# Kernel optimization log

Hardware: AMD Instinct MI355X
Metric: run time of the kernel (lower is better)

## Reference

```python
import jax, jax.numpy as jnp
import numpy as np

HIDDEN = 300
ATOM_FDIM = 133
BOND_ONLY_FDIM = 14
BOND_FDIM = ATOM_FDIM + BOND_ONLY_FDIM  # 147, chemprop concatenates atom feats into bond feats
DEPTH = 3
N_ATOMS = 100000
N_BONDS = 200000  # directed bonds, stored as reverse pairs (2k, 2k+1)
MAX_NB = 6
N_MOLS = 2000


def _lin(key, fan_in, fan_out):
    s = 1.0 / np.sqrt(fan_in)
    return jax.random.uniform(key, (fan_in, fan_out), jnp.float32, -s, s)


def setup_inputs() -> dict:
    key = jax.random.key(0)
    ks = jax.random.split(key, 16)
    f_atoms = jax.random.normal(ks[0], (N_ATOMS, ATOM_FDIM), jnp.float32)
    f_bonds = jax.random.normal(ks[1], (N_BONDS, BOND_FDIM), jnp.float32)
    a2b = jax.random.randint(ks[2], (N_ATOMS, MAX_NB), 0, N_BONDS, jnp.int32)
    b2a = jax.random.randint(ks[3], (N_BONDS,), 0, N_ATOMS, jnp.int32)
    b2revb = jnp.arange(N_BONDS, dtype=jnp.int32) ^ 1  # reverse-bond pairing
    graph_idx = jnp.sort(jax.random.randint(ks[4], (N_ATOMS,), 0, N_MOLS, jnp.int32))
    params = dict(
        W_i=_lin(ks[5], BOND_FDIM, HIDDEN),              # no bias in chemprop W_i
        W_h=_lin(ks[6], HIDDEN, HIDDEN),                 # no bias in chemprop W_h
        W_o=_lin(ks[7], ATOM_FDIM + HIDDEN, HIDDEN),
        b_o=jnp.zeros((HIDDEN,), jnp.float32),
        W_node=_lin(ks[8], HIDDEN, ATOM_FDIM),
        b_node=jnp.zeros((ATOM_FDIM,), jnp.float32),
        W_edge=_lin(ks[9], HIDDEN, BOND_ONLY_FDIM),
        b_edge=jnp.zeros((BOND_ONLY_FDIM,), jnp.float32),
        W_g1=_lin(ks[10], HIDDEN, HIDDEN),
        b_g1=jnp.zeros((HIDDEN,), jnp.float32),
        W_g2=_lin(ks[11], HIDDEN, 1),
        b_g2=jnp.zeros((1,), jnp.float32),
    )
    return dict(f_atoms=f_atoms, f_bonds=f_bonds, a2b=a2b, b2a=b2a,
                b2revb=b2revb, graph_idx=graph_idx, **params)


def reference(f_atoms, f_bonds, a2b, b2a, b2revb, graph_idx,
              W_i, W_h, W_o, b_o, W_node, b_node,
              W_edge, b_edge, W_g1, b_g1, W_g2, b_g2):
    # ---- chemprop bond-message MPN encoder (dropout=0) ----
    inp = f_bonds @ W_i                       # [n_bonds, H]
    msg = jax.nn.relu(inp)
    for _ in range(DEPTH - 1):
        a_msg = msg[a2b].sum(axis=1)          # gather neighbor bond msgs -> [n_atoms, H]
        msg = jax.nn.relu(inp + (a_msg[b2a] - msg[b2revb]) @ W_h)
    a_msg = msg[a2b].sum(axis=1)
    atom_hiddens = jax.nn.relu(jnp.concatenate([f_atoms, a_msg], axis=-1) @ W_o + b_o)
    # ---- graph pooling: per-molecule SUM (as in the forward loop) ----
    graph_emb = jax.ops.segment_sum(atom_hiddens, graph_idx, num_segments=N_MOLS)
    # ---- heads ----
    node_preds = atom_hiddens @ W_node + b_node
    # bond loop: visits each reverse pair once (even bond first), averages endpoint atoms
    e1 = jnp.arange(0, N_BONDS, 2)
    a1 = b2a[e1]
    a2 = b2a[b2revb[e1]]
    h_avg = 0.5 * (atom_hiddens[a1] + atom_hiddens[a2])
    edge_preds = h_avg @ W_edge + b_edge
    graph_preds = jax.nn.relu(graph_emb @ W_g1 + b_g1) @ W_g2 + b_g2
    return node_preds, edge_preds, graph_preds
```

## Files before the change

kernel.cpp:

```cpp
#include <hip/hip_runtime.h>

typedef unsigned short u16;
typedef unsigned int u32;

#define N_ATOMS 100000
#define N_BONDS 200000
#define N_EDGES 100000
#define HIDDEN 300
#define HP 320
#define ATOM_FDIM 133
#define BOND_FDIM 147
#define CATP 448
#define N_MOLS 2000

typedef __bf16 bf16x8 __attribute__((ext_vector_type(8)));
typedef float f32x4 __attribute__((ext_vector_type(4)));

__device__ __forceinline__ u16 f2bf(float f) {
    union { float f; u32 u; } x; x.f = f;
    u32 u = x.u;
    u32 r = u + 0x7fffu + ((u >> 16) & 1u);
    return (u16)(r >> 16);
}
__device__ __forceinline__ float bf2f(u16 h) {
    union { u32 u; float f; } x; x.u = ((u32)h) << 16;
    return x.f;
}

union U8 { uint4 v; u16 h[8]; };
union U4 { uint2 v; u16 h[4]; };

template<int ASRC, int EP, int KSTEPS>
__global__ __launch_bounds__(256, 4) void k_gemm_lds(
    const float* __restrict__ fsrc, const u16* __restrict__ src16,
    const u16* __restrict__ src16b, const int* __restrict__ i1,
    const int* __restrict__ i2, int lda, int M,
    const u16* __restrict__ Bt, int ldb,
    int Nout, float* __restrict__ Cf, int ldc,
    const float* __restrict__ bias, u16* __restrict__ O1,
    const u16* __restrict__ inp_in)
{
    constexpr int CHPR = KSTEPS * 4;
    constexpr int MASK = (CHPR % 8 == 0) ? 7 : 3;
    __shared__ __align__(16) u16 As[32 * CHPR * 8];

    const int tid = threadIdx.x;
    const int row0 = blockIdx.x * 32;

    constexpr int TOT = 32 * CHPR;
    constexpr int ITER = (TOT + 255) / 256;
#pragma unroll
    for (int it = 0; it < ITER; it++) {
        int ch = tid + it * 256;
        if (TOT % 256 != 0 && ch >= TOT) break;
        int r = ch / CHPR, c = ch - r * CHPR;
        int row = row0 + r; if (row >= M) row = M - 1;
        U8 u;
        if constexpr (ASRC == 1) {
            size_t fb = (size_t)row * lda;
#pragma unroll
            for (int e = 0; e < 8; e++) {
                int col = c * 8 + e;
                u.h[e] = (col < lda) ? f2bf(fsrc[fb + col]) : (u16)0;
            }
        } else if constexpr (ASRC == 2) {
            U8 x, y;
            x.v = *(const uint4*)(src16  + (size_t)i1[row] * HP + c * 8);
            y.v = *(const uint4*)(src16b + (size_t)i2[row] * HP + c * 8);
#pragma unroll
            for (int e = 0; e < 8; e++)
                u.h[e] = f2bf(bf2f(x.h[e]) - fmaxf(bf2f(y.h[e]), 0.f));
        } else {
            if (c < 38) {
                u.v = *(const uint4*)(src16 + (size_t)row * HP + c * 8);
            } else {
                size_t fb = (size_t)row * ATOM_FDIM;
#pragma unroll
                for (int e = 0; e < 8; e++) {
                    int col = c * 8 + e - 304;
                    u.h[e] = (col >= 0 && col < ATOM_FDIM) ? f2bf(fsrc[fb + col]) : (u16)0;
                }
            }
        }
        *(uint4*)&As[(size_t)(r * CHPR + (c ^ (r & MASK))) * 8] = u.v;
    }
    __syncthreads();

    const int lane = tid & 63;
    const int w = tid >> 6;
    const int ncol0 = w * 80;
    const int lrow = lane & 15;
    const int g = lane >> 4;
    const int lkb = g * 8;
    const int xr = lrow & MASK;

    const u16* pb[5];
#pragma unroll
    for (int n = 0; n < 5; n++)
        pb[n] = Bt + (size_t)(ncol0 + n * 16 + lrow) * ldb + lkb;

    f32x4 acc[2][5] = {};
    bf16x8 bcur[5], bnxt[5];
#pragma unroll
    for (int n = 0; n < 5; n++) bcur[n] = *(const bf16x8*)(pb[n]);

#pragma unroll
    for (int ks = 0; ks < KSTEPS; ks++) {
        if (ks + 1 < KSTEPS) {
#pragma unroll
            for (int n = 0; n < 5; n++) bnxt[n] = *(const bf16x8*)(pb[n] + (ks + 1) * 32);
        }
        const int sw = (ks * 4 + g) ^ xr;
        bf16x8 a0 = *(const bf16x8*)&As[(size_t)(lrow * CHPR + sw) * 8];
        bf16x8 a1 = *(const bf16x8*)&As[(size_t)((lrow + 16) * CHPR + sw) * 8];
#pragma unroll
        for (int n = 0; n < 5; n++) {
            acc[0][n] = __builtin_amdgcn_mfma_f32_16x16x32_bf16(bcur[n], a0, acc[0][n], 0, 0, 0);
            acc[1][n] = __builtin_amdgcn_mfma_f32_16x16x32_bf16(bcur[n], a1, acc[1][n], 0, 0, 0);
        }
#pragma unroll
        for (int n = 0; n < 5; n++) bcur[n] = bnxt[n];
    }

#pragma unroll
    for (int m = 0; m < 2; m++) {
        const int row = row0 + m * 16 + lrow;
#pragma unroll
        for (int n = 0; n < 5; n++) {
            const int colb = ncol0 + n * 16 + g * 4;
            U4 o;
            if constexpr (EP == 1) {
#pragma unroll
                for (int q = 0; q < 4; q++) o.h[q] = f2bf(acc[m][n][q]);
            } else if constexpr (EP == 2) {
                U4 ii; ii.v = *(const uint2*)&inp_in[(size_t)row * HP + colb];
#pragma unroll
                for (int q = 0; q < 4; q++) o.h[q] = f2bf(acc[m][n][q] + bf2f(ii.h[q]));
            } else {
#pragma unroll
                for (int q = 0; q < 4; q++) {
                    float x = acc[m][n][q] + ((colb + q) < Nout ? bias[colb + q] : 0.f);
                    o.h[q] = f2bf(fmaxf(x, 0.f));
                }
            }
            *(uint2*)&O1[(size_t)row * HP + colb] = o.v;
        }
    }
}

template<int ASRC, int EP, int KSTEPS, int NFW, int WAVEM>
__global__ __launch_bounds__(256) void k_gemm(
    const float* __restrict__ fsrc, const u16* __restrict__ src16,
    const u16* __restrict__ src16b, const int* __restrict__ i1,
    const int* __restrict__ i2, int lda, int M,
    const u16* __restrict__ Bt, int ldb,
    int Nout, float* __restrict__ Cf, int ldc,
    const float* __restrict__ bias, u16* __restrict__ O1,
    const u16* __restrict__ inp_in)
{
    const int tid = threadIdx.x;
    const int lane = tid & 63;
    const int w = tid >> 6;
    const int lrow = lane & 15;
    const int lkb = (lane >> 4) * 8;

    int row0, ncol0;
    if constexpr (WAVEM) { row0 = blockIdx.x * 128 + w * 32; ncol0 = 0; }
    else                 { row0 = blockIdx.x * 32;           ncol0 = w * (NFW * 16); }

    const u16* pa[2] = {nullptr, nullptr};
    const u16* pa2[2] = {nullptr, nullptr};
#pragma unroll
    for (int m = 0; m < 2; m++) {
        int r = row0 + m * 16 + lrow; if (r >= M) r = M - 1;
        if constexpr (ASRC == 0) pa[m] = src16 + (size_t)r * lda + lkb;
        if constexpr (ASRC == 4) {
            int e = 2 * r;
            pa[m]  = src16 + (size_t)i1[e] * HP + lkb;
            pa2[m] = src16 + (size_t)i1[i2[e]] * HP + lkb;
        }
    }

    const u16* pb[NFW];
#pragma unroll
    for (int n = 0; n < NFW; n++)
        pb[n] = Bt + (size_t)(ncol0 + n * 16 + lrow) * ldb + lkb;

    auto loadAfrag = [&](int m, int k0) -> bf16x8 {
        U8 u;
        if constexpr (ASRC == 0) {
            u.v = *(const uint4*)(pa[m] + k0);
        } else {
            U8 x, y; x.v = *(const uint4*)(pa[m] + k0); y.v = *(const uint4*)(pa2[m] + k0);
#pragma unroll
            for (int e = 0; e < 8; e++)
                u.h[e] = f2bf(0.5f * (bf2f(x.h[e]) + bf2f(y.h[e])));
        }
        return *(bf16x8*)&u;
    };

    f32x4 acc[2][NFW] = {};

#pragma unroll
    for (int ks = 0; ks < KSTEPS; ks++) {
        const int k0 = ks * 32;
        bf16x8 a0 = loadAfrag(0, k0);
        bf16x8 a1 = loadAfrag(1, k0);
        bf16x8 bfr[NFW];
#pragma unroll
        for (int n = 0; n < NFW; n++) bfr[n] = *(const bf16x8*)(pb[n] + k0);
#pragma unroll
        for (int n = 0; n < NFW; n++) {
            acc[0][n] = __builtin_amdgcn_mfma_f32_16x16x32_bf16(a0, bfr[n], acc[0][n], 0, 0, 0);
            acc[1][n] = __builtin_amdgcn_mfma_f32_16x16x32_bf16(a1, bfr[n], acc[1][n], 0, 0, 0);
        }
    }

    const int orow = (lane >> 4) * 4;
    const int ocol = lane & 15;
#pragma unroll
    for (int m = 0; m < 2; m++) {
#pragma unroll
        for (int n = 0; n < NFW; n++) {
#pragma unroll
            for (int q = 0; q < 4; q++) {
                int grow = row0 + m * 16 + orow + q;
                int gcol = ncol0 + n * 16 + ocol;
                float v = acc[m][n][q];
                if constexpr (EP == 0) {
                    if (grow < M && gcol < Nout)
                        Cf[(size_t)grow * ldc + gcol] = v + bias[gcol];
                } else {
                    if (grow < M) O1[(size_t)grow * HP + gcol] = f2bf(v);
                }
            }
        }
    }
}

__global__ void k_pack_wt(const float* __restrict__ W, u16* __restrict__ Bt,
                          int K, int N, int Kp, int Np)
{
    int idx = blockIdx.x * 256 + threadIdx.x;
    if (idx >= Np * Kp) return;
    int n = idx / Kp, k = idx - n * Kp;
    Bt[idx] = (n < N && k < K) ? f2bf(W[(size_t)k * N + n]) : (u16)0;
}

__global__ void k_pack_wo(const float* __restrict__ W, u16* __restrict__ Bt)
{
    int idx = blockIdx.x * 256 + threadIdx.x;
    if (idx >= 320 * CATP) return;
    int n = idx / CATP, k = idx - n * CATP;
    float v = 0.f;
    if (n < HIDDEN) {
        if (k < HIDDEN) v = W[(size_t)(ATOM_FDIM + k) * HIDDEN + n];
        else if (k >= 304 && k < 304 + ATOM_FDIM) v = W[(size_t)(k - 304) * HIDDEN + n];
    }
    Bt[idx] = f2bf(v);
}

__global__ __launch_bounds__(256) void k_aggregate(const u16* __restrict__ h,
    const int* __restrict__ a2b, u16* __restrict__ amsg)
{
    int idx = blockIdx.x * 256 + threadIdx.x;
    if (idx >= N_ATOMS * 40) return;
    int a = idx / 40, c = (idx - a * 40) * 8;
    float s[8] = {};
#pragma unroll
    for (int j = 0; j < 6; j++) {
        int b = a2b[a * 6 + j];
        U8 u; u.v = *(const uint4*)&h[(size_t)b * HP + c];
#pragma unroll
        for (int i = 0; i < 8; i++) s[i] += fmaxf(bf2f(u.h[i]), 0.f);
    }
    U8 o;
#pragma unroll
    for (int i = 0; i < 8; i++) o.h[i] = f2bf(s[i]);
    *(uint4*)&amsg[(size_t)a * HP + c] = o.v;
}

__device__ __forceinline__ int lower_bound_i(const int* a, int n, int v) {
    int lo = 0, hi = n;
    while (lo < hi) { int mid = (lo + hi) >> 1; if (a[mid] < v) lo = mid + 1; else hi = mid; }
    return lo;
}
__global__ __launch_bounds__(320) void k_segsum(const u16* __restrict__ ah,
    const int* __restrict__ gidx, float* __restrict__ gemb)
{
    int g = blockIdx.x;
    int c = threadIdx.x;
    int s = lower_bound_i(gidx, N_ATOMS, g);
    int e = lower_bound_i(gidx, N_ATOMS, g + 1);
    float sum = 0.f;
    for (int a = s; a < e; a++) sum += bf2f(ah[(size_t)a * HP + c]);
    gemb[(size_t)g * HP + c] = sum;
}

__global__ __launch_bounds__(320) void k_g1(const float* __restrict__ gemb,
    const float* __restrict__ W, const float* __restrict__ b, float* __restrict__ gh)
{
    int g = blockIdx.x, j = threadIdx.x;
    float acc = 0.f;
    if (j < HIDDEN) {
        acc = b[j];
        for (int k = 0; k < HIDDEN; k++)
            acc = fmaf(gemb[(size_t)g * HP + k], W[(size_t)k * HIDDEN + j], acc);
        acc = fmaxf(acc, 0.f);
    }
    gh[(size_t)g * HP + j] = (j < HIDDEN) ? acc : 0.f;
}
__global__ __launch_bounds__(64) void k_g2(const float* __restrict__ gh,
    const float* __restrict__ W, const float* __restrict__ b, float* __restrict__ out)
{
    int g = blockIdx.x, l = threadIdx.x;
    float acc = 0.f;
    for (int j = l; j < HIDDEN; j += 64) acc += gh[(size_t)g * HP + j] * W[j];
#pragma unroll
    for (int off = 32; off; off >>= 1) acc += __shfl_down(acc, off, 64);
    if (l == 0) out[g] = acc + b[0];
}

extern "C" void kernel_launch(void* const* d_in, const int* in_sizes, int n_in,
                              void* d_out, int out_size, void* d_ws, size_t ws_size,
                              hipStream_t stream)
{
    const float* f_atoms = (const float*)d_in[0];
    const float* f_bonds = (const float*)d_in[1];
    const int* a2b    = (const int*)d_in[2];
    const int* b2a    = (const int*)d_in[3];
    const int* b2revb = (const int*)d_in[4];
    const int* gidx   = (const int*)d_in[5];
    const float* W_i    = (const float*)d_in[6];
    const float* W_h    = (const float*)d_in[7];
    const float* W_o    = (const float*)d_in[8];
    const float* b_o    = (const float*)d_in[9];
    const float* W_node = (const float*)d_in[10];
    const float* b_node = (const float*)d_in[11];
    const float* W_edge = (const float*)d_in[12];
    const float* b_edge = (const float*)d_in[13];
    const float* W_g1   = (const float*)d_in[14];
    const float* b_g1   = (const float*)d_in[15];
    const float* W_g2   = (const float*)d_in[16];
    const float* b_g2   = (const float*)d_in[17];

    char* ws = (char*)d_ws;
    u16* inp  = (u16*)(ws + 0);
    u16* hA   = (u16*)(ws + 128000000);
    u16* hB   = (u16*)(ws + 256000000);
    u16* amsg = (u16*)(ws + 384000000);
    u16* wt_i = (u16*)(ws + 448000000);
    u16* wt_h = (u16*)(ws + 448200000);
    u16* wt_o = (u16*)(ws + 448500000);
    u16* wt_n = (u16*)(ws + 448800000);
    u16* wt_e = (u16*)(ws + 449000000);
    float* gemb = (float*)(ws + 449300000);
    float* gh   = (float*)(ws + 452000000);

    float* out_node  = (float*)d_out;
    float* out_edge  = out_node + (size_t)N_ATOMS * ATOM_FDIM;
    float* out_graph = out_node + 14700000;

    dim3 blk(256);

    k_pack_wt<<<(320 * 160 + 255) / 256, blk, 0, stream>>>(W_i, wt_i, BOND_FDIM, HIDDEN, 160, 320);
    k_pack_wt<<<(320 * 320 + 255) / 256, blk, 0, stream>>>(W_h, wt_h, HIDDEN, HIDDEN, 320, 320);
    k_pack_wo<<<(320 * CATP + 255) / 256, blk, 0, stream>>>(W_o, wt_o);
    k_pack_wt<<<(192 * 320 + 255) / 256, blk, 0, stream>>>(W_node, wt_n, HIDDEN, ATOM_FDIM, 320, 192);
    k_pack_wt<<<(64 * 320 + 255) / 256, blk, 0, stream>>>(W_edge, wt_e, HIDDEN, 14, 320, 64);

    const int gB32 = (N_BONDS + 31) / 32;
    const int gA32 = (N_ATOMS + 31) / 32;
    const int gE128 = (N_EDGES + 127) / 128;
    const int gAg = (N_ATOMS * 40 + 255) / 256;

    k_gemm_lds<1, 1, 5><<<gB32, blk, 0, stream>>>(
        f_bonds, nullptr, nullptr, nullptr, nullptr, BOND_FDIM, N_BONDS,
        wt_i, 160, 0, nullptr, 0, nullptr, inp, nullptr);

    const u16* hcur = inp;
    u16* houts[2] = { hA, hB };
    for (int d = 0; d < 2; ++d) {
        k_aggregate<<<gAg, blk, 0, stream>>>(hcur, a2b, amsg);
        k_gemm_lds<2, 2, 10><<<gB32, blk, 0, stream>>>(
            nullptr, amsg, hcur, b2a, b2revb, 0, N_BONDS,
            wt_h, 320, 0, nullptr, 0, nullptr, houts[d], inp);
        hcur = houts[d];
    }

    k_aggregate<<<gAg, blk, 0, stream>>>(hcur, a2b, amsg);
    u16* ah = hA;
    k_gemm_lds<3, 3, 14><<<gA32, blk, 0, stream>>>(
        f_atoms, amsg, nullptr, nullptr, nullptr, 0, N_ATOMS,
        wt_o, CATP, HIDDEN, nullptr, 0, b_o, ah, nullptr);

    k_gemm<0, 0, 10, 3, 0><<<gA32, blk, 0, stream>>>(
        nullptr, ah, nullptr, nullptr, nullptr, HP, N_ATOMS,
        wt_n, 320, ATOM_FDIM, out_node, ATOM_FDIM, b_node, nullptr, nullptr);

    k_gemm<4, 0, 10, 1, 1><<<gE128, blk, 0, stream>>>(
        nullptr, ah, nullptr, b2a, b2revb, 0, N_EDGES,
        wt_e, 320, 14, out_edge, 14, b_edge, nullptr, nullptr);

    k_segsum<<<N_MOLS, 320, 0, stream>>>(ah, gidx, gemb);
    k_g1<<<N_MOLS, 320, 0, stream>>>(gemb, W_g1, b_g1, gh);
    k_g2<<<N_MOLS, 64, 0, stream>>>(gh, W_g2, b_g2, out_graph);
}
```

Measured before the change: 1.150 ms.

## Warp-specialize GEMMs into persistent producer/consumer kernels with double-buffered LDS

Replaces the one-tile-per-block LDS GEMM with a persistent 512-thread kernel. Four producer waves stage the next 32-row A tile (gathers, subtract-relu) into a second LDS buffer while four MFMA waves compute the current tile, so global loads overlap with compute. To make producer loads plain vector copies, f_bonds and f_atoms are first converted to padded bf16 buffers by new pack kernels. This adds two extra full passes over the feature matrices and doubles LDS use, and with a fixed grid of 512 only one tile is ever staged ahead.

```diff
diff --git a/kernel.cpp b/kernel.cpp
--- a/kernel.cpp
+++ b/kernel.cpp
@@ -30,120 +30,157 @@
 union U8 { uint4 v; u16 h[8]; };
 union U4 { uint2 v; u16 h[4]; };
 
-template<int ASRC, int EP, int KSTEPS>
-__global__ __launch_bounds__(256, 4) void k_gemm_lds(
-    const float* __restrict__ fsrc, const u16* __restrict__ src16,
-    const u16* __restrict__ src16b, const int* __restrict__ i1,
-    const int* __restrict__ i2, int lda, int M,
-    const u16* __restrict__ Bt, int ldb,
-    int Nout, float* __restrict__ Cf, int ldc,
-    const float* __restrict__ bias, u16* __restrict__ O1,
-    const u16* __restrict__ inp_in)
+template<int ASRC, int EP, int KSTEPS, int LDA>
+__global__ __launch_bounds__(512, 4) void k_gemm_pipe(
+    const u16* __restrict__ srcA, const u16* __restrict__ srcB,
+    const int* __restrict__ i1, const int* __restrict__ i2,
+    int ntiles, const u16* __restrict__ Bt, int ldb,
+    int Nout, const float* __restrict__ bias,
+    u16* __restrict__ O1, const u16* __restrict__ inp_in)
 {
     constexpr int CHPR = KSTEPS * 4;
     constexpr int MASK = (CHPR % 8 == 0) ? 7 : 3;
-    __shared__ __align__(16) u16 As[32 * CHPR * 8];
+    constexpr int CPT = (CHPR + 7) / 8;
+    __shared__ __align__(16) u16 As[2][32 * CHPR * 8];
 
     const int tid = threadIdx.x;
-    const int row0 = blockIdx.x * 32;
-
-    constexpr int TOT = 32 * CHPR;
-    constexpr int ITER = (TOT + 255) / 256;
-#pragma unroll
-    for (int it = 0; it < ITER; it++) {
-        int ch = tid + it * 256;
-        if (TOT % 256 != 0 && ch >= TOT) break;
-        int r = ch / CHPR, c = ch - r * CHPR;
-        int row = row0 + r; if (row >= M) row = M - 1;
-        U8 u;
-        if constexpr (ASRC == 1) {
-            size_t fb = (size_t)row * lda;
-#pragma unroll
-            for (int e = 0; e < 8; e++) {
-                int col = c * 8 + e;
-                u.h[e] = (col < lda) ? f2bf(fsrc[fb + col]) : (u16)0;
+    const int wv = tid >> 6;
+    const int tile0 = blockIdx.x;
+    if (tile0 >= ntiles) return;
+
+    if (wv >= 4) {
+        const int ptid = tid - 256;
+        const int rr = ptid >> 3;
+        const int c0 = ptid & 7;
+
+        uint4 sx[CPT], sy[(ASRC == 2) ? CPT : 1];
+
+        auto stage = [&](int tile, int buf) {
+            const int row = tile * 32 + rr;
+            if constexpr (ASRC == 0) {
+                const u16* px = srcA + (size_t)row * LDA;
+#pragma unroll
+                for (int j = 0; j < CPT; j++) {
+                    int c = c0 + 8 * j;
+                    if (CHPR % 8 == 0 || c < CHPR)
+                        sx[j] = *(const uint4*)(px + c * 8);
+                }
+            } else if constexpr (ASRC == 2) {
+                const u16* px = srcA + (size_t)i1[row] * HP;
+                const u16* py = srcB + (size_t)i2[row] * HP;
+#pragma unroll
+                for (int j = 0; j < CPT; j++) {
+                    int c = c0 + 8 * j;
+                    sx[j] = *(const uint4*)(px + c * 8);
+                    sy[j] = *(const uint4*)(py + c * 8);
+                }
+            } else {
+                const u16* pa = srcA + (size_t)row * HP;
+                const u16* pf = srcB + (size_t)row * 160;
+#pragma unroll
+                for (int j = 0; j < CPT; j++) {
+                    int c = c0 + 8 * j;
+                    sx[j] = (c < 38) ? *(const uint4*)(pa + c * 8)
+                                     : *(const uint4*)(pf + (c - 38) * 8);
+                }
             }
-        } else if constexpr (ASRC == 2) {
-            U8 x, y;
-            x.v = *(const uint4*)(src16  + (size_t)i1[row] * HP + c * 8);
-            y.v = *(const uint4*)(src16b + (size_t)i2[row] * HP + c * 8);
-#pragma unroll
-            for (int e = 0; e < 8; e++)
-                u.h[e] = f2bf(bf2f(x.h[e]) - fmaxf(bf2f(y.h[e]), 0.f));
-        } else {
-            if (c < 38) {
-                u.v = *(const uint4*)(src16 + (size_t)row * HP + c * 8);
-            } else {
-                size_t fb = (size_t)row * ATOM_FDIM;
-#pragma unroll
-                for (int e = 0; e < 8; e++) {
-                    int col = c * 8 + e - 304;
-                    u.h[e] = (col >= 0 && col < ATOM_FDIM) ? f2bf(fsrc[fb + col]) : (u16)0;
-                }
+#pragma unroll
+            for (int j = 0; j < CPT; j++) {
+                int c = c0 + 8 * j;
+                if (CHPR % 8 != 0 && c >= CHPR) continue;
+                U8 u;
+                if constexpr (ASRC == 2) {
+                    U8 x, y; x.v = sx[j]; y.v = sy[j];
+#pragma unroll
+                    for (int e = 0; e < 8; e++)
+                        u.h[e] = f2bf(bf2f(x.h[e]) - fmaxf(bf2f(y.h[e]), 0.f));
+                } else {
+                    u.v = sx[j];
+                }
+                *(uint4*)&As[buf][(size_t)(rr * CHPR + (c ^ (rr & MASK))) * 8] = u.v;
             }
-        }
-        *(uint4*)&As[(size_t)(r * CHPR + (c ^ (r & MASK))) * 8] = u.v;
-    }
-    __syncthreads();
-
-    const int lane = tid & 63;
-    const int w = tid >> 6;
-    const int ncol0 = w * 80;
-    const int lrow = lane & 15;
-    const int g = lane >> 4;
-    const int lkb = g * 8;
-    const int xr = lrow & MASK;
-
-    const u16* pb[5];
-#pragma unroll
-    for (int n = 0; n < 5; n++)
-        pb[n] = Bt + (size_t)(ncol0 + n * 16 + lrow) * ldb + lkb;
-
-    f32x4 acc[2][5] = {};
-    bf16x8 bcur[5], bnxt[5];
-#pragma unroll
-    for (int n = 0; n < 5; n++) bcur[n] = *(const bf16x8*)(pb[n]);
-
-#pragma unroll
-    for (int ks = 0; ks < KSTEPS; ks++) {
-        if (ks + 1 < KSTEPS) {
-#pragma unroll
-            for (int n = 0; n < 5; n++) bnxt[n] = *(const bf16x8*)(pb[n] + (ks + 1) * 32);
-        }
-        const int sw = (ks * 4 + g) ^ xr;
-        bf16x8 a0 = *(const bf16x8*)&As[(size_t)(lrow * CHPR + sw) * 8];
-        bf16x8 a1 = *(const bf16x8*)&As[(size_t)((lrow + 16) * CHPR + sw) * 8];
-#pragma unroll
-        for (int n = 0; n < 5; n++) {
-            acc[0][n] = __builtin_amdgcn_mfma_f32_16x16x32_bf16(bcur[n], a0, acc[0][n], 0, 0, 0);
-            acc[1][n] = __builtin_amdgcn_mfma_f32_16x16x32_bf16(bcur[n], a1, acc[1][n], 0, 0, 0);
-        }
-#pragma unroll
-        for (int n = 0; n < 5; n++) bcur[n] = bnxt[n];
-    }
-
-#pragma unroll
-    for (int m = 0; m < 2; m++) {
-        const int row = row0 + m * 16 + lrow;
-#pragma unroll
-        for (int n = 0; n < 5; n++) {
-            const int colb = ncol0 + n * 16 + g * 4;
-            U4 o;
-            if constexpr (EP == 1) {
-#pragma unroll
-                for (int q = 0; q < 4; q++) o.h[q] = f2bf(acc[m][n][q]);
-            } else if constexpr (EP == 2) {
-                U4 ii; ii.v = *(const uint2*)&inp_in[(size_t)row * HP + colb];
-#pragma unroll
-                for (int q = 0; q < 4; q++) o.h[q] = f2bf(acc[m][n][q] + bf2f(ii.h[q]));
-            } else {
-#pragma unroll
-                for (int q = 0; q < 4; q++) {
-                    float x = acc[m][n][q] + ((colb + q) < Nout ? bias[colb + q] : 0.f);
-                    o.h[q] = f2bf(fmaxf(x, 0.f));
-                }
+        };
+
+        stage(tile0, 0);
+        __syncthreads();
+        int cur = 0;
+        for (int tile = tile0;;) {
+            int nxt = tile + gridDim.x;
+            if (nxt >= ntiles) break;
+            stage(nxt, cur ^ 1);
+            __syncthreads();
+            cur ^= 1; tile = nxt;
+        }
+    } else {
+        const int lane = tid & 63;
+        const int ncol0 = wv * 80;
+        const int lrow = lane & 15;
+        const int g = lane >> 4;
+        const int lkb = g * 8;
+        const int xr = lrow & MASK;
+
+        const u16* pb[5];
+#pragma unroll
+        for (int n = 0; n < 5; n++)
+            pb[n] = Bt + (size_t)(ncol0 + n * 16 + lrow) * ldb + lkb;
+
+        auto compute = [&](int tile, int buf) {
+            f32x4 acc[2][5] = {};
+            bf16x8 bcur[5], bnxt[5];
+#pragma unroll
+            for (int n = 0; n < 5; n++) bcur[n] = *(const bf16x8*)(pb[n]);
+#pragma unroll
+            for (int ks = 0; ks < KSTEPS; ks++) {
+                if (ks + 1 < KSTEPS) {
+#pragma unroll
+                    for (int n = 0; n < 5; n++) bnxt[n] = *(const bf16x8*)(pb[n] + (ks + 1) * 32);
+                }
+                const int sw = (ks * 4 + g) ^ xr;
+                bf16x8 a0 = *(const bf16x8*)&As[buf][(size_t)(lrow * CHPR + sw) * 8];
+                bf16x8 a1 = *(const bf16x8*)&As[buf][(size_t)((lrow + 16) * CHPR + sw) * 8];
+#pragma unroll
+                for (int n = 0; n < 5; n++) {
+                    acc[0][n] = __builtin_amdgcn_mfma_f32_16x16x32_bf16(bcur[n], a0, acc[0][n], 0, 0, 0);
+                    acc[1][n] = __builtin_amdgcn_mfma_f32_16x16x32_bf16(bcur[n], a1, acc[1][n], 0, 0, 0);
+                }
+#pragma unroll
+                for (int n = 0; n < 5; n++) bcur[n] = bnxt[n];
             }
-            *(uint2*)&O1[(size_t)row * HP + colb] = o.v;
+            const int row0 = tile * 32;
+#pragma unroll
+            for (int m = 0; m < 2; m++) {
+                const int row = row0 + m * 16 + lrow;
+#pragma unroll
+                for (int n = 0; n < 5; n++) {
+                    const int colb = ncol0 + n * 16 + g * 4;
+                    U4 o;
+                    if constexpr (EP == 1) {
+#pragma unroll
+                        for (int q = 0; q < 4; q++) o.h[q] = f2bf(acc[m][n][q]);
+                    } else if constexpr (EP == 2) {
+                        U4 ii; ii.v = *(const uint2*)&inp_in[(size_t)row * HP + colb];
+#pragma unroll
+                        for (int q = 0; q < 4; q++) o.h[q] = f2bf(acc[m][n][q] + bf2f(ii.h[q]));
+                    } else {
+#pragma unroll
+                        for (int q = 0; q < 4; q++) {
+                            float x = acc[m][n][q] + ((colb + q) < Nout ? bias[colb + q] : 0.f);
+                            o.h[q] = f2bf(fmaxf(x, 0.f));
+                        }
+                    }
+                    *(uint2*)&O1[(size_t)row * HP + colb] = o.v;
+                }
+            }
+        };
+
+        __syncthreads();
+        int cur = 0;
+        for (int tile = tile0;;) {
+            int nxt = tile + gridDim.x;
+            compute(tile, cur);
+            if (nxt >= ntiles) break;
+            __syncthreads();
+            cur ^= 1; tile = nxt;
         }
     }
 }
@@ -258,6 +295,22 @@
         else if (k >= 304 && k < 304 + ATOM_FDIM) v = W[(size_t)(k - 304) * HIDDEN + n];
     }
     Bt[idx] = f2bf(v);
+}
+
+__global__ void k_pack_bonds(const float* __restrict__ fb, u16* __restrict__ out)
+{
+    int idx = blockIdx.x * 256 + threadIdx.x;
+    if (idx >= N_BONDS * 160) return;
+    int b = idx / 160, c = idx - b * 160;
+    out[idx] = (c < BOND_FDIM) ? f2bf(fb[(size_t)b * BOND_FDIM + c]) : (u16)0;
+}
+
+__global__ void k_pack_fa(const float* __restrict__ fa, u16* __restrict__ out)
+{
+    int idx = blockIdx.x * 256 + threadIdx.x;
+    if (idx >= N_ATOMS * 160) return;
+    int a = idx / 160, c = idx - a * 160;
+    out[idx] = (c < ATOM_FDIM) ? f2bf(fa[(size_t)a * ATOM_FDIM + c]) : (u16)0;
 }
 
 __global__ __launch_bounds__(256) void k_aggregate(const u16* __restrict__ h,
@@ -362,6 +415,7 @@
     float* out_graph = out_node + 14700000;
 
     dim3 blk(256);
+    dim3 blk512(512);
 
     k_pack_wt<<<(320 * 160 + 255) / 256, blk, 0, stream>>>(W_i, wt_i, BOND_FDIM, HIDDEN, 160, 320);
     k_pack_wt<<<(320 * 320 + 255) / 256, blk, 0, stream>>>(W_h, wt_h, HIDDEN, HIDDEN, 320, 320);
@@ -369,30 +423,38 @@
     k_pack_wt<<<(192 * 320 + 255) / 256, blk, 0, stream>>>(W_node, wt_n, HIDDEN, ATOM_FDIM, 320, 192);
     k_pack_wt<<<(64 * 320 + 255) / 256, blk, 0, stream>>>(W_edge, wt_e, HIDDEN, 14, 320, 64);
 
-    const int gB32 = (N_BONDS + 31) / 32;
+    const int ntB = N_BONDS / 32;
+    const int ntA = N_ATOMS / 32;
+    const int GP = 512;
     const int gA32 = (N_ATOMS + 31) / 32;
     const int gE128 = (N_EDGES + 127) / 128;
     const int gAg = (N_ATOMS * 40 + 255) / 256;
 
-    k_gemm_lds<1, 1, 5><<<gB32, blk, 0, stream>>>(
-        f_bonds, nullptr, nullptr, nullptr, nullptr, BOND_FDIM, N_BONDS,
-        wt_i, 160, 0, nullptr, 0, nullptr, inp, nullptr);
+    u16* fbpack = hB;
+    k_pack_bonds<<<(N_BONDS * 160 + 255) / 256, blk, 0, stream>>>(f_bonds, fbpack);
+
+    k_gemm_pipe<0, 1, 5, 160><<<GP, blk512, 0, stream>>>(
+        fbpack, nullptr, nullptr, nullptr, ntB,
+        wt_i, 160, 0, nullptr, inp, nullptr);
 
     const u16* hcur = inp;
     u16* houts[2] = { hA, hB };
     for (int d = 0; d < 2; ++d) {
         k_aggregate<<<gAg, blk, 0, stream>>>(hcur, a2b, amsg);
-        k_gemm_lds<2, 2, 10><<<gB32, blk, 0, stream>>>(
-            nullptr, amsg, hcur, b2a, b2revb, 0, N_BONDS,
-            wt_h, 320, 0, nullptr, 0, nullptr, houts[d], inp);
+        k_gemm_pipe<2, 2, 10, 0><<<GP, blk512, 0, stream>>>(
+            amsg, hcur, b2a, b2revb, ntB,
+            wt_h, 320, 0, nullptr, houts[d], inp);
         hcur = houts[d];
     }
 
     k_aggregate<<<gAg, blk, 0, stream>>>(hcur, a2b, amsg);
+    u16* fapack = hB;
+    k_pack_fa<<<(N_ATOMS * 160 + 255) / 256, blk, 0, stream>>>(f_atoms, fapack);
+
     u16* ah = hA;
-    k_gemm_lds<3, 3, 14><<<gA32, blk, 0, stream>>>(
-        f_atoms, amsg, nullptr, nullptr, nullptr, 0, N_ATOMS,
-        wt_o, CATP, HIDDEN, nullptr, 0, b_o, ah, nullptr);
+    k_gemm_pipe<3, 3, 14, 0><<<GP, blk512, 0, stream>>>(
+        amsg, fapack, nullptr, nullptr, ntA,
+        wt_o, CATP, HIDDEN, b_o, ah, nullptr);
 
     k_gemm<0, 0, 10, 3, 0><<<gA32, blk, 0, stream>>>(
         nullptr, ah, nullptr, nullptr, nullptr, HP, N_ATOMS,
```

Measured after the change: 1.525 ms. 1.33x slower.

## Fuse node and edge heads by projecting atoms before averaging endpoints

Applied to the files above, without the earlier changes.

The edge head is rewritten using linearity: every atom is projected through a combined node+edge weight matrix once, and each edge output then averages the two endpoint projections. This replaces the separate gather-and-average GEMM, and the node and edge heads now share a single LDS GEMM. The A-tile load is also restructured to one row per 8 threads, the residual `inp` read is hoisted ahead of the barrier, B fragments are prefetched two steps ahead, and the b2revb gather is replaced by row^1. In exchange, edge outputs are computed in a different order, the code now depends on the b2revb pairing and on the row counts dividing exactly by 32, and there is an extra small kernel plus an intermediate buffer.

```diff
diff --git a/kernel.cpp b/kernel.cpp
--- a/kernel.cpp
+++ b/kernel.cpp
@@ -32,63 +32,71 @@
 
 template<int ASRC, int EP, int KSTEPS>
 __global__ __launch_bounds__(256, 4) void k_gemm_lds(
-    const float* __restrict__ fsrc, const u16* __restrict__ src16,
-    const u16* __restrict__ src16b, const int* __restrict__ i1,
-    const int* __restrict__ i2, int lda, int M,
-    const u16* __restrict__ Bt, int ldb,
-    int Nout, float* __restrict__ Cf, int ldc,
-    const float* __restrict__ bias, u16* __restrict__ O1,
+    const u16* __restrict__ srcA, const u16* __restrict__ srcB,
+    const float* __restrict__ fsrc, const int* __restrict__ i1,
+    const u16* __restrict__ Bt, int ldb, int Nout,
+    const float* __restrict__ bias, const float* __restrict__ bias2,
+    u16* __restrict__ O1, float* __restrict__ F1, float* __restrict__ F2,
     const u16* __restrict__ inp_in)
 {
     constexpr int CHPR = KSTEPS * 4;
     constexpr int MASK = (CHPR % 8 == 0) ? 7 : 3;
+    constexpr int CPT = (CHPR + 7) / 8;
     __shared__ __align__(16) u16 As[32 * CHPR * 8];
 
     const int tid = threadIdx.x;
     const int row0 = blockIdx.x * 32;
 
-    constexpr int TOT = 32 * CHPR;
-    constexpr int ITER = (TOT + 255) / 256;
-#pragma unroll
-    for (int it = 0; it < ITER; it++) {
-        int ch = tid + it * 256;
-        if (TOT % 256 != 0 && ch >= TOT) break;
-        int r = ch / CHPR, c = ch - r * CHPR;
-        int row = row0 + r; if (row >= M) row = M - 1;
-        U8 u;
-        if constexpr (ASRC == 1) {
-            size_t fb = (size_t)row * lda;
-#pragma unroll
-            for (int e = 0; e < 8; e++) {
-                int col = c * 8 + e;
-                u.h[e] = (col < lda) ? f2bf(fsrc[fb + col]) : (u16)0;
-            }
-        } else if constexpr (ASRC == 2) {
-            U8 x, y;
-            x.v = *(const uint4*)(src16  + (size_t)i1[row] * HP + c * 8);
-            y.v = *(const uint4*)(src16b + (size_t)i2[row] * HP + c * 8);
-#pragma unroll
-            for (int e = 0; e < 8; e++)
-                u.h[e] = f2bf(bf2f(x.h[e]) - fmaxf(bf2f(y.h[e]), 0.f));
-        } else {
-            if (c < 38) {
-                u.v = *(const uint4*)(src16 + (size_t)row * HP + c * 8);
+    {
+        const int rr = tid >> 3;
+        const int cc = tid & 7;
+        const int row = row0 + rr;
+        const u16* px = nullptr; const u16* py = nullptr; const float* pf = nullptr;
+        if constexpr (ASRC == 0) px = srcA + (size_t)row * HP;
+        if constexpr (ASRC == 1) pf = fsrc + (size_t)row * BOND_FDIM;
+        if constexpr (ASRC == 2) {
+            px = srcA + (size_t)i1[row] * HP;
+            py = srcB + (size_t)(row ^ 1) * HP;
+        }
+        if constexpr (ASRC == 3) { px = srcA + (size_t)row * HP; pf = fsrc + (size_t)row * ATOM_FDIM; }
+#pragma unroll
+        for (int j = 0; j < CPT; j++) {
+            const int c = cc + 8 * j;
+            if (CPT * 8 != CHPR && c >= CHPR) continue;
+            U8 u;
+            if constexpr (ASRC == 0) {
+                u.v = *(const uint4*)(px + c * 8);
+            } else if constexpr (ASRC == 1) {
+#pragma unroll
+                for (int e = 0; e < 8; e++) {
+                    int col = c * 8 + e;
+                    u.h[e] = (col < BOND_FDIM) ? f2bf(pf[col]) : (u16)0;
+                }
+            } else if constexpr (ASRC == 2) {
+                U8 x, y;
+                x.v = *(const uint4*)(px + c * 8);
+                y.v = *(const uint4*)(py + c * 8);
+#pragma unroll
+                for (int e = 0; e < 8; e++)
+                    u.h[e] = f2bf(bf2f(x.h[e]) - fmaxf(bf2f(y.h[e]), 0.f));
             } else {
-                size_t fb = (size_t)row * ATOM_FDIM;
-#pragma unroll
-                for (int e = 0; e < 8; e++) {
-                    int col = c * 8 + e - 304;
-                    u.h[e] = (col >= 0 && col < ATOM_FDIM) ? f2bf(fsrc[fb + col]) : (u16)0;
+                if (c < 38) {
+                    u.v = *(const uint4*)(px + c * 8);
+                } else {
+#pragma unroll
+                    for (int e = 0; e < 8; e++) {
+                        int col = c * 8 + e - 304;
+                        u.h[e] = (col >= 0 && col < ATOM_FDIM) ? f2bf(pf[col]) : (u16)0;
+                    }
                 }
             }
-        }
-        *(uint4*)&As[(size_t)(r * CHPR + (c ^ (r & MASK))) * 8] = u.v;
-    }
-    __syncthreads();
+            *(uint4*)&As[(size_t)(rr * CHPR + (c ^ (rr & MASK))) * 8] = u.v;
+        }
+    }
 
     const int lane = tid & 63;
-    const int w = tid >> 6;
-    const int ncol0 = w * 80;
+    const int wv = tid >> 6;
+    const int ncol0 = wv * 80;
     const int lrow = lane & 15;
     const int g = lane >> 4;
     const int lkb = g * 8;
@@ -99,27 +107,42 @@
     for (int n = 0; n < 5; n++)
         pb[n] = Bt + (size_t)(ncol0 + n * 16 + lrow) * ldb + lkb;
 
+    U4 ii[10];
+    if constexpr (EP == 2) {
+#pragma unroll
+        for (int m = 0; m < 2; m++)
+#pragma unroll
+            for (int n = 0; n < 5; n++)
+                ii[m * 5 + n].v = *(const uint2*)&inp_in[
+                    (size_t)(row0 + m * 16 + lrow) * HP + ncol0 + n * 16 + g * 4];
+    }
+
+    __syncthreads();
+
     f32x4 acc[2][5] = {};
-    bf16x8 bcur[5], bnxt[5];
-#pragma unroll
-    for (int n = 0; n < 5; n++) bcur[n] = *(const bf16x8*)(pb[n]);
+    bf16x8 bb[3][5];
+#pragma unroll
+    for (int n = 0; n < 5; n++) bb[0][n] = *(const bf16x8*)(pb[n]);
+    if constexpr (KSTEPS > 1) {
+#pragma unroll
+        for (int n = 0; n < 5; n++) bb[1][n] = *(const bf16x8*)(pb[n] + 32);
+    }
 
 #pragma unroll
     for (int ks = 0; ks < KSTEPS; ks++) {
-        if (ks + 1 < KSTEPS) {
-#pragma unroll
-            for (int n = 0; n < 5; n++) bnxt[n] = *(const bf16x8*)(pb[n] + (ks + 1) * 32);
+        if (ks + 2 < KSTEPS) {
+#pragma unroll
+            for (int n = 0; n < 5; n++)
+                bb[(ks + 2) % 3][n] = *(const bf16x8*)(pb[n] + (ks + 2) * 32);
         }
         const int sw = (ks * 4 + g) ^ xr;
         bf16x8 a0 = *(const bf16x8*)&As[(size_t)(lrow * CHPR + sw) * 8];
         bf16x8 a1 = *(const bf16x8*)&As[(size_t)((lrow + 16) * CHPR + sw) * 8];
 #pragma unroll
         for (int n = 0; n < 5; n++) {
-            acc[0][n] = __builtin_amdgcn_mfma_f32_16x16x32_bf16(bcur[n], a0, acc[0][n], 0, 0, 0);
-            acc[1][n] = __builtin_amdgcn_mfma_f32_16x16x32_bf16(bcur[n], a1, acc[1][n], 0, 0, 0);
-        }
-#pragma unroll
-        for (int n = 0; n < 5; n++) bcur[n] = bnxt[n];
+            acc[0][n] = __builtin_amdgcn_mfma_f32_16x16x32_bf16(bb[ks % 3][n], a0, acc[0][n], 0, 0, 0);
+            acc[1][n] = __builtin_amdgcn_mfma_f32_16x16x32_bf16(bb[ks % 3][n], a1, acc[1][n], 0, 0, 0);
+        }
     }
 
 #pragma unroll
@@ -128,111 +151,31 @@
 #pragma unroll
         for (int n = 0; n < 5; n++) {
             const int colb = ncol0 + n * 16 + g * 4;
-            U4 o;
-            if constexpr (EP == 1) {
-#pragma unroll
-                for (int q = 0; q < 4; q++) o.h[q] = f2bf(acc[m][n][q]);
-            } else if constexpr (EP == 2) {
-                U4 ii; ii.v = *(const uint2*)&inp_in[(size_t)row * HP + colb];
-#pragma unroll
-                for (int q = 0; q < 4; q++) o.h[q] = f2bf(acc[m][n][q] + bf2f(ii.h[q]));
+            if constexpr (EP == 4) {
+                if (colb >= 148) continue;
+#pragma unroll
+                for (int q = 0; q < 4; q++) {
+                    const int col = colb + q;
+                    const float v = acc[m][n][q];
+                    if (col < 133) F1[(size_t)row * 133 + col] = v + bias[col];
+                    else if (col < 147) F2[(size_t)row * 16 + (col - 133)] = v + bias2[col - 133];
+                }
             } else {
-#pragma unroll
-                for (int q = 0; q < 4; q++) {
-                    float x = acc[m][n][q] + ((colb + q) < Nout ? bias[colb + q] : 0.f);
-                    o.h[q] = f2bf(fmaxf(x, 0.f));
+                U4 o;
+                if constexpr (EP == 1) {
+#pragma unroll
+                    for (int q = 0; q < 4; q++) o.h[q] = f2bf(acc[m][n][q]);
+                } else if constexpr (EP == 2) {
+#pragma unroll
+                    for (int q = 0; q < 4; q++) o.h[q] = f2bf(acc[m][n][q] + bf2f(ii[m * 5 + n].h[q]));
+                } else {
+#pragma unroll
+                    for (int q = 0; q < 4; q++) {
+                        float x = acc[m][n][q] + ((colb + q) < Nout ? bias[colb + q] : 0.f);
+                        o.h[q] = f2bf(fmaxf(x, 0.f));
+                    }
                 }
-            }
-            *(uint2*)&O1[(size_t)row * HP + colb] = o.v;
-        }
-    }
-}
-
-template<int ASRC, int EP, int KSTEPS, int NFW, int WAVEM>
-__global__ __launch_bounds__(256) void k_gemm(
-    const float* __restrict__ fsrc, const u16* __restrict__ src16,
-    const u16* __restrict__ src16b, const int* __restrict__ i1,
-    const int* __restrict__ i2, int lda, int M,
-    const u16* __restrict__ Bt, int ldb,
-    int Nout, float* __restrict__ Cf, int ldc,
-    const float* __restrict__ bias, u16* __restrict__ O1,
-    const u16* __restrict__ inp_in)
-{
-    const int tid = threadIdx.x;
-    const int lane = tid & 63;
-    const int w = tid >> 6;
-    const int lrow = lane & 15;
-    const int lkb = (lane >> 4) * 8;
-
-    int row0, ncol0;
-    if constexpr (WAVEM) { row0 = blockIdx.x * 128 + w * 32; ncol0 = 0; }
-    else                 { row0 = blockIdx.x * 32;           ncol0 = w * (NFW * 16); }
-
-    const u16* pa[2] = {nullptr, nullptr};
-    const u16* pa2[2] = {nullptr, nullptr};
-#pragma unroll
-    for (int m = 0; m < 2; m++) {
-        int r = row0 + m * 16 + lrow; if (r >= M) r = M - 1;
-        if constexpr (ASRC == 0) pa[m] = src16 + (size_t)r * lda + lkb;
-        if constexpr (ASRC == 4) {
-            int e = 2 * r;
-            pa[m]  = src16 + (size_t)i1[e] * HP + lkb;
-            pa2[m] = src16 + (size_t)i1[i2[e]] * HP + lkb;
-        }
-    }
-
-    const u16* pb[NFW];
-#pragma unroll
-    for (int n = 0; n < NFW; n++)
-        pb[n] = Bt + (size_t)(ncol0 + n * 16 + lrow) * ldb + lkb;
-
-    auto loadAfrag = [&](int m, int k0) -> bf16x8 {
-        U8 u;
-        if constexpr (ASRC == 0) {
-            u.v = *(const uint4*)(pa[m] + k0);
-        } else {
-            U8 x, y; x.v = *(const uint4*)(pa[m] + k0); y.v = *(const uint4*)(pa2[m] + k0);
-#pragma unroll
-            for (int e = 0; e < 8; e++)
-                u.h[e] = f2bf(0.5f * (bf2f(x.h[e]) + bf2f(y.h[e])));
-        }
-        return *(bf16x8*)&u;
-    };
-
-    f32x4 acc[2][NFW] = {};
-
-#pragma unroll
-    for (int ks = 0; ks < KSTEPS; ks++) {
-        const int k0 = ks * 32;
-        bf16x8 a0 = loadAfrag(0, k0);
-        bf16x8 a1 = loadAfrag(1, k0);
-        bf16x8 bfr[NFW];
-#pragma unroll
-        for (int n = 0; n < NFW; n++) bfr[n] = *(const bf16x8*)(pb[n] + k0);
-#pragma unroll
-        for (int n = 0; n < NFW; n++) {
-            acc[0][n] = __builtin_amdgcn_mfma_f32_16x16x32_bf16(a0, bfr[n], acc[0][n], 0, 0, 0);
-            acc[1][n] = __builtin_amdgcn_mfma_f32_16x16x32_bf16(a1, bfr[n], acc[1][n], 0, 0, 0);
-        }
-    }
-
-    const int orow = (lane >> 4) * 4;
-    const int ocol = lane & 15;
-#pragma unroll
-    for (int m = 0; m < 2; m++) {
-#pragma unroll
-        for (int n = 0; n < NFW; n++) {
-#pragma unroll
-            for (int q = 0; q < 4; q++) {
-                int grow = row0 + m * 16 + orow + q;
-                int gcol = ncol0 + n * 16 + ocol;
-                float v = acc[m][n][q];
-                if constexpr (EP == 0) {
-                    if (grow < M && gcol < Nout)
-                        Cf[(size_t)grow * ldc + gcol] = v + bias[gcol];
-                } else {
-                    if (grow < M) O1[(size_t)grow * HP + gcol] = f2bf(v);
-                }
+                *(uint2*)&O1[(size_t)row * HP + colb] = o.v;
             }
         }
     }
@@ -260,6 +203,20 @@
     Bt[idx] = f2bf(v);
 }
 
+__global__ void k_pack_wne(const float* __restrict__ Wn, const float* __restrict__ We,
+                           u16* __restrict__ Bt)
+{
+    int idx = blockIdx.x * 256 + threadIdx.x;
+    if (idx >= 320 * 320) return;
+    int n = idx / 320, k = idx - n * 320;
+    float v = 0.f;
+    if (k < HIDDEN) {
+        if (n < ATOM_FDIM) v = Wn[(size_t)k * ATOM_FDIM + n];
+        else if (n < ATOM_FDIM + 14) v = We[(size_t)k * 14 + (n - ATOM_FDIM)];
+    }
+    Bt[idx] = f2bf(v);
+}
+
 __global__ __launch_bounds__(256) void k_aggregate(const u16* __restrict__ h,
     const int* __restrict__ a2b, u16* __restrict__ amsg)
 {
@@ -278,6 +235,19 @@
 #pragma unroll
     for (int i = 0; i < 8; i++) o.h[i] = f2bf(s[i]);
     *(uint4*)&amsg[(size_t)a * HP + c] = o.v;
+}
+
+__global__ __launch_bounds__(256) void k_edge(const float* __restrict__ E,
+    const int* __restrict__ b2a, float* __restrict__ out)
+{
+    int idx = blockIdx.x * 256 + threadIdx.x;
+    if (idx >= N_EDGES * 7) return;
+    int e = idx / 7, p = idx - e * 7;
+    int a1 = b2a[2 * e], a2 = b2a[2 * e + 1];
+    float2 x = *(const float2*)&E[(size_t)a1 * 16 + 2 * p];
+    float2 y = *(const float2*)&E[(size_t)a2 * 16 + 2 * p];
+    float2 o; o.x = 0.5f * (x.x + y.x); o.y = 0.5f * (x.y + y.y);
+    *(float2*)&out[(size_t)e * 14 + 2 * p] = o;
 }
 
 __device__ __forceinline__ int lower_bound_i(const int* a, int n, int v) {
@@ -329,7 +299,6 @@
     const float* f_bonds = (const float*)d_in[1];
     const int* a2b    = (const int*)d_in[2];
     const int* b2a    = (const int*)d_in[3];
-    const int* b2revb = (const int*)d_in[4];
     const int* gidx   = (const int*)d_in[5];
     const float* W_i    = (const float*)d_in[6];
     const float* W_h    = (const float*)d_in[7];
@@ -345,15 +314,14 @@
     const float* b_g2   = (const float*)d_in[17];
 
     char* ws = (char*)d_ws;
-    u16* inp  = (u16*)(ws + 0);
-    u16* hA   = (u16*)(ws + 128000000);
-    u16* hB   = (u16*)(ws + 256000000);
-    u16* amsg = (u16*)(ws + 384000000);
-    u16* wt_i = (u16*)(ws + 448000000);
-    u16* wt_h = (u16*)(ws + 448200000);
-    u16* wt_o = (u16*)(ws + 448500000);
-    u16* wt_n = (u16*)(ws + 448800000);
-    u16* wt_e = (u16*)(ws + 449000000);
+    u16* inp   = (u16*)(ws + 0);
+    u16* hA    = (u16*)(ws + 128000000);
+    u16* hB    = (u16*)(ws + 256000000);
+    u16* amsg  = (u16*)(ws + 384000000);
+    u16* wt_i  = (u16*)(ws + 448000000);
+    u16* wt_h  = (u16*)(ws + 448200000);
+    u16* wt_o  = (u16*)(ws + 448500000);
+    u16* wt_ne = (u16*)(ws + 448800000);
     float* gemb = (float*)(ws + 449300000);
     float* gh   = (float*)(ws + 452000000);
 
@@ -366,41 +334,38 @@
     k_pack_wt<<<(320 * 160 + 255) / 256, blk, 0, stream>>>(W_i, wt_i, BOND_FDIM, HIDDEN, 160, 320);
     k_pack_wt<<<(320 * 320 + 255) / 256, blk, 0, stream>>>(W_h, wt_h, HIDDEN, HIDDEN, 320, 320);
     k_pack_wo<<<(320 * CATP + 255) / 256, blk, 0, stream>>>(W_o, wt_o);
-    k_pack_wt<<<(192 * 320 + 255) / 256, blk, 0, stream>>>(W_node, wt_n, HIDDEN, ATOM_FDIM, 320, 192);
-    k_pack_wt<<<(64 * 320 + 255) / 256, blk, 0, stream>>>(W_edge, wt_e, HIDDEN, 14, 320, 64);
-
-    const int gB32 = (N_BONDS + 31) / 32;
-    const int gA32 = (N_ATOMS + 31) / 32;
-    const int gE128 = (N_EDGES + 127) / 128;
+    k_pack_wne<<<(320 * 320 + 255) / 256, blk, 0, stream>>>(W_node, W_edge, wt_ne);
+
+    const int gB32 = N_BONDS / 32;
+    const int gA32 = N_ATOMS / 32;
     const int gAg = (N_ATOMS * 40 + 255) / 256;
 
     k_gemm_lds<1, 1, 5><<<gB32, blk, 0, stream>>>(
-        f_bonds, nullptr, nullptr, nullptr, nullptr, BOND_FDIM, N_BONDS,
-        wt_i, 160, 0, nullptr, 0, nullptr, inp, nullptr);
+        nullptr, nullptr, f_bonds, nullptr,
+        wt_i, 160, 0, nullptr, nullptr, inp, nullptr, nullptr, nullptr);
 
     const u16* hcur = inp;
     u16* houts[2] = { hA, hB };
     for (int d = 0; d < 2; ++d) {
         k_aggregate<<<gAg, blk, 0, stream>>>(hcur, a2b, amsg);
         k_gemm_lds<2, 2, 10><<<gB32, blk, 0, stream>>>(
-            nullptr, amsg, hcur, b2a, b2revb, 0, N_BONDS,
-            wt_h, 320, 0, nullptr, 0, nullptr, houts[d], inp);
+            amsg, hcur, nullptr, b2a,
+            wt_h, 320, 0, nullptr, nullptr, houts[d], nullptr, nullptr, inp);
         hcur = houts[d];
     }
 
     k_aggregate<<<gAg, blk, 0, stream>>>(hcur, a2b, amsg);
     u16* ah = hA;
     k_gemm_lds<3, 3, 14><<<gA32, blk, 0, stream>>>(
-        f_atoms, amsg, nullptr, nullptr, nullptr, 0, N_ATOMS,
-        wt_o, CATP, HIDDEN, nullptr, 0, b_o, ah, nullptr);
-
-    k_gemm<0, 0, 10, 3, 0><<<gA32, blk, 0, stream>>>(
-        nullptr, ah, nullptr, nullptr, nullptr, HP, N_ATOMS,
-        wt_n, 320, ATOM_FDIM, out_node, ATOM_FDIM, b_node, nullptr, nullptr);
-
-    k_gemm<4, 0, 10, 1, 1><<<gE128, blk, 0, stream>>>(
-        nullptr, ah, nullptr, b2a, b2revb, 0, N_EDGES,
-        wt_e, 320, 14, out_edge, 14, b_edge, nullptr, nullptr);
+        amsg, nullptr, f_atoms, nullptr,
+        wt_o, CATP, HIDDEN, b_o, nullptr, ah, nullptr, nullptr, nullptr);
+
+    float* Ebuf = (float*)hB;
+    k_gemm_lds<0, 4, 10><<<gA32, blk, 0, stream>>>(
+        ah, nullptr, nullptr, nullptr,
+        wt_ne, 320, 0, b_node, b_edge, nullptr, out_node, Ebuf, nullptr);
+
+    k_edge<<<(N_EDGES * 7 + 255) / 256, blk, 0, stream>>>(Ebuf, b2a, out_edge);
 
     k_segsum<<<N_MOLS, 320, 0, stream>>>(ah, gidx, gemb);
     k_g1<<<N_MOLS, 320, 0, stream>>>(gemb, W_g1, b_g1, gh);
```

New measurement: 1.084 ms. 5.7% less time.
